# Performance work log

Measured on AMD Instinct MI355X. Metric: run time of the kernel, lower is better.

Reference implementation:

```python
import jax, jax.numpy as jnp
import numpy as np

B, T, C = 4, 2048, 768   # batch, seq, n_embd
E, K = 8, 2              # n_routed_experts, moe_top_k (expert hidden dim == C per source)


def setup_inputs() -> dict:
    key = jax.random.key(0)
    ks = jax.random.split(key, 6)
    s = 0.02  # init scale to keep relu(x)^2 well-behaved
    return {
        "x": jax.random.normal(ks[0], (B, T, C), jnp.float32),
        "w_fc_sh": jax.random.normal(ks[1], (C, C), jnp.float32) * s,    # shared expert c_fc (stored [in,out])
        "w_proj_sh": jax.random.normal(ks[2], (C, C), jnp.float32) * s,  # shared expert c_proj
        "w1": jax.random.normal(ks[3], (E, C, C), jnp.float32) * s,      # routed experts c_fc, [E,in,out]
        "w2": jax.random.normal(ks[4], (E, C, C), jnp.float32) * s,      # routed experts c_proj
        "router_w": jax.random.normal(ks[5], (E, C), jnp.float32) * s,   # router weight [E, C]
        "balance_bias": jnp.zeros((E,), jnp.float32),                    # router balance_bias buffer
    }


def _mlp(x, wfc, wproj):
    # MLP: c_proj(relu(c_fc(x))**2)
    h = jnp.square(jax.nn.relu(x @ wfc))
    return h @ wproj


def reference(x, w_fc_sh, w_proj_sh, w1, w2, router_w, balance_bias):
    Bx, Tx, Cx = x.shape
    shared = _mlp(x, w_fc_sh, w_proj_sh)                    # [B,T,C]

    xf = x.reshape(-1, Cx)                                  # [N,C]
    # --- router ---
    logits = xf.astype(jnp.float32) @ router_w.T            # [N,E]
    scores = jax.nn.sigmoid(logits)
    _, idx = jax.lax.top_k(scores + balance_bias, K)        # selection uses biased scores
    tw = jnp.take_along_axis(scores, idx, axis=-1)          # gate weights from unbiased scores
    tw = tw / (tw.sum(-1, keepdims=True) + 1e-20)           # [N,K]

    # per-token per-expert combine weights (equivalent to gather/MLP/index_add loop)
    combine = (jax.nn.one_hot(idx, E, dtype=tw.dtype) * tw[..., None]).sum(1)  # [N,E]

    # dense all-expert compute, masked combine (same math as sparse dispatch)
    h = jnp.square(jax.nn.relu(jnp.einsum('nc,ech->neh', xf, w1)))  # [N,E,H]
    y = jnp.einsum('neh,ehc->nec', h, w2)                            # [N,E,C]
    routed = jnp.einsum('nec,ne->nc', y, combine)                    # [N,C]

    return shared + routed.reshape(Bx, Tx, Cx)
```

## Files before the change

kernel.cpp:

```cpp
#include <hip/hip_runtime.h>
#include <stdint.h>

#define N_TOK 8192
#define C_DIM 768
#define E_NUM 8
#define NTK 24
#define GRIDG 624
#define PREP_WT 10368
#define PREP_TOT (PREP_WT + N_TOK / 4)

typedef short short8 __attribute__((ext_vector_type(8)));
typedef __bf16 bf16x8 __attribute__((ext_vector_type(8)));
typedef float f32x4 __attribute__((ext_vector_type(4)));

static __device__ __forceinline__ unsigned short f2bf(float f) {
    unsigned u = __float_as_uint(f);
    unsigned r = u + 0x7FFFu + ((u >> 16) & 1u);
    return (unsigned short)(r >> 16);
}
static __device__ __forceinline__ float bf2f(unsigned short h) {
    return __uint_as_float(((unsigned)h) << 16);
}

__global__ __launch_bounds__(256) void prep_kernel(const float* __restrict__ wfc,
                                                   const float* __restrict__ wpj,
                                                   const float* __restrict__ w1,
                                                   const float* __restrict__ w2,
                                                   unsigned short* __restrict__ Wt,
                                                   const float* __restrict__ x,
                                                   const float* __restrict__ rw,
                                                   const float* __restrict__ bias,
                                                   float* __restrict__ topk_w,
                                                   int* __restrict__ eids,
                                                   unsigned short* __restrict__ xb) {
    __shared__ float tile[32][33];
    const int bx = blockIdx.x;
    const int t = threadIdx.x;
    if (bx < PREP_WT) {
        const int m = bx / 576;
        const int rem = bx - m * 576;
        const int i0 = (rem / 24) * 32;
        const int o0 = (rem % 24) * 32;
        const int tx = t & 31, ty = t >> 5;
        const float* src = (m == 0) ? wfc : (m == 1) ? wpj
                         : (m < 10) ? (w1 + (size_t)(m - 2) * C_DIM * C_DIM)
                                    : (w2 + (size_t)(m - 10) * C_DIM * C_DIM);
        #pragma unroll
        for (int rr = 0; rr < 32; rr += 8)
            tile[ty + rr][tx] = src[(size_t)(i0 + ty + rr) * C_DIM + o0 + tx];
        __syncthreads();
        unsigned short* dst = Wt + (size_t)m * C_DIM * C_DIM;
        #pragma unroll
        for (int rr = 0; rr < 32; rr += 8) {
            int o = o0 + ty + rr;
            dst[(size_t)o * C_DIM + i0 + tx] = f2bf(tile[tx][ty + rr]);
        }
    } else {
        const int rb = bx - PREP_WT;
        const int wave = t >> 6;
        const int lane = t & 63;
        const int n = rb * 4 + wave;
        const float* xp = x + (size_t)n * C_DIM + lane * 12;
        float xv[12];
        #pragma unroll
        for (int j = 0; j < 12; j++) xv[j] = xp[j];
        unsigned short* xbp = xb + (size_t)n * C_DIM + lane * 12;
        #pragma unroll
        for (int j = 0; j < 12; j++) xbp[j] = f2bf(xv[j]);
        float acc[E_NUM];
        #pragma unroll
        for (int e = 0; e < E_NUM; e++) acc[e] = 0.f;
        #pragma unroll
        for (int e = 0; e < E_NUM; e++) {
            const float* wp = rw + (size_t)e * C_DIM + lane * 12;
            #pragma unroll
            for (int j = 0; j < 12; j++) acc[e] += xv[j] * wp[j];
        }
        #pragma unroll
        for (int e = 0; e < E_NUM; e++) {
            #pragma unroll
            for (int off = 32; off > 0; off >>= 1) acc[e] += __shfl_xor(acc[e], off, 64);
        }
        if (lane == 0) {
            float sc[E_NUM];
            #pragma unroll
            for (int e = 0; e < E_NUM; e++) sc[e] = 1.f / (1.f + expf(-acc[e]));
            int e0 = 0; float best = -1e30f;
            #pragma unroll
            for (int e = 0; e < E_NUM; e++) { float v = sc[e] + bias[e]; if (v > best) { best = v; e0 = e; } }
            int e1 = -1; float best1 = -1e30f;
            #pragma unroll
            for (int e = 0; e < E_NUM; e++) { if (e == e0) continue; float v = sc[e] + bias[e]; if (v > best1) { best1 = v; e1 = e; } }
            float w0 = sc[e0], w1 = sc[e1];
            float s = w0 + w1 + 1e-20f;
            w0 /= s; w1 /= s;
            topk_w[n * 2] = w0; topk_w[n * 2 + 1] = w1;
            eids[n * 2] = e0; eids[n * 2 + 1] = e1;
        }
    }
}

__global__ __launch_bounds__(1024) void bucketize_kernel(const int* __restrict__ eids,
                                                         int* __restrict__ counts,
                                                         int* __restrict__ buckets) {
    const int e = blockIdx.x;
    const int t = threadIdx.x;
    const int wv = t >> 6, lane = t & 63;
    __shared__ int wave_tot[16];
    int running = 0;
    for (int start = 0; start < 2 * N_TOK; start += 1024) {
        const int i = start + t;
        const int f = (eids[i] == e) ? 1 : 0;
        unsigned long long mask = __ballot(f);
        int pre = __popcll(mask & ((1ull << lane) - 1ull));
        if (lane == 0) wave_tot[wv] = __popcll(mask);
        __syncthreads();
        int wbase = 0, tot = 0;
        #pragma unroll
        for (int j = 0; j < 16; j++) { int c = wave_tot[j]; tot += c; if (j < wv) wbase += c; }
        if (f) buckets[e * N_TOK + running + wbase + pre] = i;
        running += tot;
        __syncthreads();
    }
    if (t == 0) counts[e] = running;
}

#define GLOAD_LDS(g, l) __builtin_amdgcn_global_load_lds((const __attribute__((address_space(1))) void*)(g), (__attribute__((address_space(3))) void*)(l), 16, 0, 0)
#define WAITVM(n) asm volatile("s_waitcnt vmcnt(" #n ")" ::: "memory")
#define SCHEDB() __builtin_amdgcn_sched_barrier(0)
#define BAR() __builtin_amdgcn_s_barrier()

template <int PHASE>
__global__ __launch_bounds__(512, 4) void gemm_all_kernel(const unsigned short* __restrict__ Adir,
                                                          const unsigned short* __restrict__ Agat,
                                                          const unsigned short* __restrict__ WtAll,
                                                          void* __restrict__ dstDir,
                                                          unsigned short* __restrict__ dstGat,
                                                          const int* __restrict__ counts,
                                                          const int* __restrict__ buckets) {
    const int fid = blockIdx.x;
    const int xcd = fid & 7;
    const int i6 = fid >> 3;
    const int xx = xcd * 13 + i6 / 6;
    const int y = i6 % 6;
    int cz[E_NUM];
    #pragma unroll
    for (int zz = 0; zz < E_NUM; zz++) cz[zz] = counts[zz];
    int xo[E_NUM + 1]; int a = 0;
    #pragma unroll
    for (int zz = 0; zz < E_NUM; zz++) { xo[zz] = a; a += (cz[zz] + 255) >> 8; }
    xo[E_NUM] = a;
    if (xx >= a + 32) return;
    const bool sh = (xx >= a);
    int z = 0, xl = xx - a;
    if (!sh) {
        #pragma unroll
        for (int zz = 0; zz < E_NUM; zz++)
            if (xx >= xo[zz] && xx < xo[zz + 1]) { z = zz; xl = xx - xo[zz]; }
    }
    const int rows = sh ? N_TOK : cz[z];
    const int r0 = xl * 256;
    const int c0 = y * 128;

    __shared__ __align__(16) unsigned short lds[3 * 12288];

    const int t = threadIdx.x;
    const int lane = t & 63;
    const int wv = t >> 6;
    const int wm = wv >> 1;
    const int wn = wv & 1;

    const int widx = sh ? (PHASE == 0 ? 0 : 1) : (PHASE == 0 ? 2 + z : 10 + z);
    const unsigned short* Bmat = WtAll + (size_t)widx * C_DIM * C_DIM;
    const int* bk = buckets + z * N_TOK;

    const int scol = (((lane & 3) ^ ((lane >> 3) & 3)) * 8);
    const int rA0 = wv * 16 + (lane >> 2);
    const int rA1 = 128 + rA0;
    int g0, g1;
    const unsigned short* Asrc;
    if (sh) {
        Asrc = Adir;
        g0 = r0 + rA0; g1 = r0 + rA1;
    } else {
        Asrc = Agat;
        int p0 = r0 + rA0, p1 = r0 + rA1;
        int e0v = bk[p0 < rows ? p0 : rows - 1];
        int e1v = bk[p1 < rows ? p1 : rows - 1];
        g0 = (PHASE == 0) ? (e0v >> 1) : e0v;
        g1 = (PHASE == 0) ? (e1v >> 1) : e1v;
    }
    const unsigned short* ap0 = Asrc + (size_t)g0 * C_DIM + scol;
    const unsigned short* ap1 = Asrc + (size_t)g1 * C_DIM + scol;
    const unsigned short* bp  = Bmat + (size_t)(c0 + rA0) * C_DIM + scol;

    f32x4 acc[4][4];
    #pragma unroll
    for (int i = 0; i < 4; i++)
        #pragma unroll
        for (int j = 0; j < 4; j++) acc[i][j] = (f32x4){0.f, 0.f, 0.f, 0.f};

    const int fr = lane & 15;
    const int fq = lane >> 4;
    const int ks = ((fq ^ ((fr >> 1) & 3)) * 8);

    #pragma unroll
    for (int p = 0; p < 2; ++p) {
        unsigned short* d = lds + p * 12288;
        const int ko = p * 32;
        GLOAD_LDS(ap0 + ko, d + wv * 512 + lane * 8);
        GLOAD_LDS(ap1 + ko, d + 4096 + wv * 512 + lane * 8);
        GLOAD_LDS(bp + ko,  d + 8192 + wv * 512 + lane * 8);
    }

    #pragma unroll
    for (int kt = 0; kt < NTK; ++kt) {
        if (kt + 1 < NTK) { WAITVM(3); }
        else              { WAITVM(0); }
        BAR();
        SCHEDB();
        if (kt + 2 < NTK) {
            unsigned short* d = lds + ((kt + 2) % 3) * 12288;
            const int ko = (kt + 2) * 32;
            GLOAD_LDS(ap0 + ko, d + wv * 512 + lane * 8);
            GLOAD_LDS(ap1 + ko, d + 4096 + wv * 512 + lane * 8);
            GLOAD_LDS(bp + ko,  d + 8192 + wv * 512 + lane * 8);
        }
        SCHEDB();
        const unsigned short* buf = lds + (kt % 3) * 12288;
        short8 afr[4], bfr[4];
        #pragma unroll
        for (int i = 0; i < 4; i++)
            afr[i] = *reinterpret_cast<const short8*>(buf + (size_t)(wm * 64 + i * 16 + fr) * 32 + ks);
        #pragma unroll
        for (int j = 0; j < 4; j++)
            bfr[j] = *reinterpret_cast<const short8*>(buf + 8192 + (size_t)(wn * 64 + j * 16 + fr) * 32 + ks);
        __builtin_amdgcn_s_setprio(1);
        #pragma unroll
        for (int i = 0; i < 4; i++)
            #pragma unroll
            for (int j = 0; j < 4; j++)
                acc[i][j] = __builtin_amdgcn_mfma_f32_16x16x32_bf16(
                    __builtin_bit_cast(bf16x8, afr[i]), __builtin_bit_cast(bf16x8, bfr[j]), acc[i][j], 0, 0, 0);
        __builtin_amdgcn_s_setprio(0);
    }

    const int orow = r0 + wm * 64;
    const int ocol = c0 + wn * 64;
    if (sh) {
        if constexpr (PHASE == 0) {
            unsigned short* Hd = (unsigned short*)dstDir;
            #pragma unroll
            for (int i = 0; i < 4; i++)
                #pragma unroll
                for (int rr = 0; rr < 4; rr++) {
                    size_t base = (size_t)(orow + i * 16 + fq * 4 + rr) * C_DIM;
                    #pragma unroll
                    for (int j = 0; j < 4; j++) {
                        float v = acc[i][j][rr];
                        float rl = v > 0.f ? v : 0.f;
                        Hd[base + ocol + j * 16 + fr] = f2bf(rl * rl);
                    }
                }
        } else {
            float* od = (float*)dstDir;
            #pragma unroll
            for (int i = 0; i < 4; i++)
                #pragma unroll
                for (int rr = 0; rr < 4; rr++) {
                    size_t base = (size_t)(orow + i * 16 + fq * 4 + rr) * C_DIM;
                    #pragma unroll
                    for (int j = 0; j < 4; j++)
                        od[base + ocol + j * 16 + fr] = acc[i][j][rr];
                }
        }
    } else {
        #pragma unroll
        for (int i = 0; i < 4; i++)
            #pragma unroll
            for (int rr = 0; rr < 4; rr++) {
                int pos = orow + i * 16 + fq * 4 + rr;
                if (pos < rows) {
                    int ent = bk[pos];
                    size_t base = (size_t)ent * C_DIM;
                    #pragma unroll
                    for (int j = 0; j < 4; j++) {
                        float v = acc[i][j][rr];
                        if (PHASE == 0) {
                            float rl = v > 0.f ? v : 0.f;
                            dstGat[base + ocol + j * 16 + fr] = f2bf(rl * rl);
                        } else {
                            dstGat[base + ocol + j * 16 + fr] = f2bf(v);
                        }
                    }
                }
            }
    }
}

__global__ void combine_kernel(float* __restrict__ out, const unsigned short* __restrict__ Y,
                               const float* __restrict__ tw) {
    int idx = blockIdx.x * blockDim.x + threadIdx.x;
    const int per_row = C_DIM / 4;
    if (idx >= N_TOK * per_row) return;
    int n = idx / per_row;
    int c = (idx % per_row) * 4;
    float w0 = tw[n * 2], w1 = tw[n * 2 + 1];
    const ushort4 a = *reinterpret_cast<const ushort4*>(Y + (size_t)(n * 2) * C_DIM + c);
    const ushort4 b = *reinterpret_cast<const ushort4*>(Y + (size_t)(n * 2 + 1) * C_DIM + c);
    float4* op = reinterpret_cast<float4*>(out + (size_t)n * C_DIM + c);
    float4 o = *op;
    o.x += w0 * bf2f(a.x) + w1 * bf2f(b.x);
    o.y += w0 * bf2f(a.y) + w1 * bf2f(b.y);
    o.z += w0 * bf2f(a.z) + w1 * bf2f(b.z);
    o.w += w0 * bf2f(a.w) + w1 * bf2f(b.w);
    *op = o;
}

extern "C" void kernel_launch(void* const* d_in, const int* in_sizes, int n_in,
                              void* d_out, int out_size, void* d_ws, size_t ws_size,
                              hipStream_t stream) {
    const float* x   = (const float*)d_in[0];
    const float* wfc = (const float*)d_in[1];
    const float* wpj = (const float*)d_in[2];
    const float* w1  = (const float*)d_in[3];
    const float* w2  = (const float*)d_in[4];
    const float* rw  = (const float*)d_in[5];
    const float* bias= (const float*)d_in[6];
    float* out = (float*)d_out;

    char* ws = (char*)d_ws;
    size_t off = 0;
    auto alloc = [&](size_t bytes) { void* p = ws + off; off += (bytes + 255) & ~(size_t)255; return p; };
    unsigned short* xb   = (unsigned short*)alloc((size_t)N_TOK * C_DIM * 2);
    unsigned short* Wt   = (unsigned short*)alloc((size_t)18 * C_DIM * C_DIM * 2);
    unsigned short* H    = (unsigned short*)alloc((size_t)N_TOK * 2 * C_DIM * 2);
    unsigned short* Hsh  = (unsigned short*)alloc((size_t)N_TOK * C_DIM * 2);
    unsigned short* Y    = (unsigned short*)alloc((size_t)N_TOK * 2 * C_DIM * 2);
    float* topk_w        = (float*)alloc((size_t)N_TOK * 2 * 4);
    int* counts          = (int*)alloc(256);
    int* buckets         = (int*)alloc((size_t)E_NUM * N_TOK * 4);
    int* eids            = (int*)alloc((size_t)2 * N_TOK * 4);

    prep_kernel<<<PREP_TOT, 256, 0, stream>>>(wfc, wpj, w1, w2, Wt, x, rw, bias, topk_w, eids, xb);
    bucketize_kernel<<<E_NUM, 1024, 0, stream>>>(eids, counts, buckets);

    gemm_all_kernel<0><<<GRIDG, 512, 0, stream>>>(xb, xb, Wt, Hsh, H, counts, buckets);
    gemm_all_kernel<1><<<GRIDG, 512, 0, stream>>>(Hsh, H, Wt, out, Y, counts, buckets);

    combine_kernel<<<(N_TOK * (C_DIM / 4) + 255) / 256, 256, 0, stream>>>(out, Y, topk_w);
}
```

Measured before the change: 131.5 us.

## Fuse gate-weighted combine into second GEMM via atomic adds, compact H layout

```diff
diff --git a/kernel.cpp b/kernel.cpp
--- a/kernel.cpp
+++ b/kernel.cpp
@@ -137,7 +137,8 @@
                                                           void* __restrict__ dstDir,
                                                           unsigned short* __restrict__ dstGat,
                                                           const int* __restrict__ counts,
-                                                          const int* __restrict__ buckets) {
+                                                          const int* __restrict__ buckets,
+                                                          const float* __restrict__ tw) {
     const int fid = blockIdx.x;
     const int xcd = fid & 7;
     const int i6 = fid >> 3;
@@ -182,13 +183,17 @@
     if (sh) {
         Asrc = Adir;
         g0 = r0 + rA0; g1 = r0 + rA1;
-    } else {
+    } else if (PHASE == 0) {
         Asrc = Agat;
         int p0 = r0 + rA0, p1 = r0 + rA1;
         int e0v = bk[p0 < rows ? p0 : rows - 1];
         int e1v = bk[p1 < rows ? p1 : rows - 1];
-        g0 = (PHASE == 0) ? (e0v >> 1) : e0v;
-        g1 = (PHASE == 0) ? (e1v >> 1) : e1v;
+        g0 = e0v >> 1;
+        g1 = e1v >> 1;
+    } else {
+        Asrc = Agat;
+        g0 = xx * 256 + rA0;
+        g1 = xx * 256 + rA1;
     }
     const unsigned short* ap0 = Asrc + (size_t)g0 * C_DIM + scol;
     const unsigned short* ap1 = Asrc + (size_t)g1 * C_DIM + scol;
@@ -245,76 +250,49 @@
         __builtin_amdgcn_s_setprio(0);
     }
 
-    const int orow = r0 + wm * 64;
+    const int orow = wm * 64;
     const int ocol = c0 + wn * 64;
-    if (sh) {
-        if constexpr (PHASE == 0) {
-            unsigned short* Hd = (unsigned short*)dstDir;
-            #pragma unroll
-            for (int i = 0; i < 4; i++)
+    if constexpr (PHASE == 0) {
+        #pragma unroll
+        for (int i = 0; i < 4; i++)
+            #pragma unroll
+            for (int rr = 0; rr < 4; rr++) {
+                int local = orow + i * 16 + fq * 4 + rr;
                 #pragma unroll
-                for (int rr = 0; rr < 4; rr++) {
-                    size_t base = (size_t)(orow + i * 16 + fq * 4 + rr) * C_DIM;
-                    #pragma unroll
-                    for (int j = 0; j < 4; j++) {
-                        float v = acc[i][j][rr];
-                        float rl = v > 0.f ? v : 0.f;
-                        Hd[base + ocol + j * 16 + fr] = f2bf(rl * rl);
-                    }
-                }
-        } else {
-            float* od = (float*)dstDir;
-            #pragma unroll
-            for (int i = 0; i < 4; i++)
-                #pragma unroll
-                for (int rr = 0; rr < 4; rr++) {
-                    size_t base = (size_t)(orow + i * 16 + fq * 4 + rr) * C_DIM;
-                    #pragma unroll
-                    for (int j = 0; j < 4; j++)
-                        od[base + ocol + j * 16 + fr] = acc[i][j][rr];
-                }
-        }
-    } else {
-        #pragma unroll
-        for (int i = 0; i < 4; i++)
-            #pragma unroll
-            for (int rr = 0; rr < 4; rr++) {
-                int pos = orow + i * 16 + fq * 4 + rr;
-                if (pos < rows) {
-                    int ent = bk[pos];
-                    size_t base = (size_t)ent * C_DIM;
-                    #pragma unroll
-                    for (int j = 0; j < 4; j++) {
-                        float v = acc[i][j][rr];
-                        if (PHASE == 0) {
-                            float rl = v > 0.f ? v : 0.f;
-                            dstGat[base + ocol + j * 16 + fr] = f2bf(rl * rl);
-                        } else {
-                            dstGat[base + ocol + j * 16 + fr] = f2bf(v);
-                        }
+                for (int j = 0; j < 4; j++) {
+                    float v = acc[i][j][rr];
+                    float rl = v > 0.f ? v : 0.f;
+                    unsigned short hv = f2bf(rl * rl);
+                    if (sh) {
+                        ((unsigned short*)dstDir)[(size_t)(r0 + local) * C_DIM + ocol + j * 16 + fr] = hv;
+                    } else if (r0 + local < rows) {
+                        dstGat[(size_t)(xx * 256 + local) * C_DIM + ocol + j * 16 + fr] = hv;
                     }
                 }
             }
-    }
-}
-
-__global__ void combine_kernel(float* __restrict__ out, const unsigned short* __restrict__ Y,
-                               const float* __restrict__ tw) {
-    int idx = blockIdx.x * blockDim.x + threadIdx.x;
-    const int per_row = C_DIM / 4;
-    if (idx >= N_TOK * per_row) return;
-    int n = idx / per_row;
-    int c = (idx % per_row) * 4;
-    float w0 = tw[n * 2], w1 = tw[n * 2 + 1];
-    const ushort4 a = *reinterpret_cast<const ushort4*>(Y + (size_t)(n * 2) * C_DIM + c);
-    const ushort4 b = *reinterpret_cast<const ushort4*>(Y + (size_t)(n * 2 + 1) * C_DIM + c);
-    float4* op = reinterpret_cast<float4*>(out + (size_t)n * C_DIM + c);
-    float4 o = *op;
-    o.x += w0 * bf2f(a.x) + w1 * bf2f(b.x);
-    o.y += w0 * bf2f(a.y) + w1 * bf2f(b.y);
-    o.z += w0 * bf2f(a.z) + w1 * bf2f(b.z);
-    o.w += w0 * bf2f(a.w) + w1 * bf2f(b.w);
-    *op = o;
+    } else {
+        float* od = (float*)dstDir;
+        #pragma unroll
+        for (int i = 0; i < 4; i++)
+            #pragma unroll
+            for (int rr = 0; rr < 4; rr++) {
+                int local = orow + i * 16 + fq * 4 + rr;
+                int pos = r0 + local;
+                if (sh) {
+                    size_t base = (size_t)pos * C_DIM;
+                    #pragma unroll
+                    for (int j = 0; j < 4; j++)
+                        unsafeAtomicAdd(&od[base + ocol + j * 16 + fr], acc[i][j][rr]);
+                } else if (pos < rows) {
+                    int ent = bk[pos];
+                    float w = tw[ent];
+                    size_t base = (size_t)(ent >> 1) * C_DIM;
+                    #pragma unroll
+                    for (int j = 0; j < 4; j++)
+                        unsafeAtomicAdd(&od[base + ocol + j * 16 + fr], w * acc[i][j][rr]);
+                }
+            }
+    }
 }
 
 extern "C" void kernel_launch(void* const* d_in, const int* in_sizes, int n_in,
@@ -334,19 +312,17 @@
     auto alloc = [&](size_t bytes) { void* p = ws + off; off += (bytes + 255) & ~(size_t)255; return p; };
     unsigned short* xb   = (unsigned short*)alloc((size_t)N_TOK * C_DIM * 2);
     unsigned short* Wt   = (unsigned short*)alloc((size_t)18 * C_DIM * C_DIM * 2);
-    unsigned short* H    = (unsigned short*)alloc((size_t)N_TOK * 2 * C_DIM * 2);
+    unsigned short* H    = (unsigned short*)alloc((size_t)80 * 256 * C_DIM * 2);
     unsigned short* Hsh  = (unsigned short*)alloc((size_t)N_TOK * C_DIM * 2);
-    unsigned short* Y    = (unsigned short*)alloc((size_t)N_TOK * 2 * C_DIM * 2);
     float* topk_w        = (float*)alloc((size_t)N_TOK * 2 * 4);
     int* counts          = (int*)alloc(256);
     int* buckets         = (int*)alloc((size_t)E_NUM * N_TOK * 4);
     int* eids            = (int*)alloc((size_t)2 * N_TOK * 4);
 
+    hipMemsetAsync(out, 0, (size_t)N_TOK * C_DIM * 4, stream);
     prep_kernel<<<PREP_TOT, 256, 0, stream>>>(wfc, wpj, w1, w2, Wt, x, rw, bias, topk_w, eids, xb);
     bucketize_kernel<<<E_NUM, 1024, 0, stream>>>(eids, counts, buckets);
 
-    gemm_all_kernel<0><<<GRIDG, 512, 0, stream>>>(xb, xb, Wt, Hsh, H, counts, buckets);
-    gemm_all_kernel<1><<<GRIDG, 512, 0, stream>>>(Hsh, H, Wt, out, Y, counts, buckets);
-
-    combine_kernel<<<(N_TOK * (C_DIM / 4) + 255) / 256, 256, 0, stream>>>(out, Y, topk_w);
-}
+    gemm_all_kernel<0><<<GRIDG, 512, 0, stream>>>(xb, xb, Wt, Hsh, H, counts, buckets, topk_w);
+    gemm_all_kernel<1><<<GRIDG, 512, 0, stream>>>(Hsh, H, Wt, out, nullptr, counts, buckets, topk_w);
+}
```

Result: slower. 170.1 us (+29.3%).
